# Performance work log

Hardware: AMD Instinct MI355X
Metric: run time of the kernel (lower is better)

## Reference

```python
import jax, jax.numpy as jnp
import numpy as np

B, LQ, LK, D = 8, 2048, 2048, 128
NEG = -100000.0


def setup_inputs() -> dict:
    key = jax.random.key(0)
    kq, kk, kv, km = jax.random.split(key, 4)
    q = jax.random.normal(kq, (B, LQ, D), dtype=jnp.float32)
    k = jax.random.normal(kk, (B, LK, D), dtype=jnp.float32)
    v = jax.random.normal(kv, (B, LK, D), dtype=jnp.float32)
    mask = jax.random.randint(km, (B, LQ, LK), 0, 2, dtype=jnp.int32)
    return {"q": q, "k": k, "v": v, "mask": mask}


def reference(q, k, v, mask):
    # atten_score = q @ k^T / sqrt(d)   [B, Lq, Lk]
    scores = jnp.einsum("bqd,bkd->bqk", q, k) / jnp.sqrt(jnp.float32(q.shape[-1]))
    # mask_mod == 2: additive mask, masked positions pushed to large negative
    scores = scores + mask.astype(jnp.float32) * NEG
    # sigmoid instead of softmax (no normalization across keys)
    attn = jax.nn.sigmoid(scores)
    return jnp.einsum("bqk,bkd->bqd", attn, v)
```

## Files before the change

### kernel.cpp

```cpp
#include <hip/hip_runtime.h>
#include <hip/hip_bf16.h>

#define B_   8
#define LQ_  2048
#define LK_  2048
#define D_   128
#define QBLK 64
#define KBLK 64
#define KSPLIT 2
#define KRANGE (LK_ / KSPLIT)
#define NT    (KRANGE / KBLK)
#define THREADS 512
#define SCALE 0.08838834764831845f

typedef __attribute__((ext_vector_type(8))) __bf16 bf16x8;
typedef __attribute__((ext_vector_type(4))) __bf16 bf16x4;
typedef __attribute__((ext_vector_type(4))) float  f32x4;
typedef __attribute__((ext_vector_type(4))) float  fx4;

#define KS_OFF 0
#define VT_OFF 8192
#define PS_OFF 16384
#define SMEM_ELEMS 21504

__global__ __launch_bounds__(THREADS, 4)
void sigattn_kernel(const float* __restrict__ q, const float* __restrict__ k,
                    const float* __restrict__ v, const int* __restrict__ mask,
                    float* __restrict__ out)
{
    __shared__ __bf16 smem[SMEM_ELEMS];

    const int tid  = threadIdx.x;
    const int lane = tid & 63;
    const int wid  = tid >> 6;
    const int qg   = wid & 3;
    const int kg   = wid >> 2;
    const int l15  = lane & 15;
    const int g    = lane >> 4;

    const int bid  = blockIdx.x;
    const int b    = bid & 7;
    const int rest = bid >> 3;
    const int q0   = (rest >> 1) * QBLK;
    const int ks   = rest & 1;

    const float* qb = q + (size_t)b * LQ_ * D_ + (size_t)q0 * D_;
    const float* kb = k + (size_t)b * LK_ * D_ + (size_t)ks * KRANGE * D_;
    const float* vb = v + (size_t)b * LK_ * D_ + (size_t)ks * KRANGE * D_;
    const int*   mb = mask + (size_t)b * LQ_ * LK_ + (size_t)q0 * LK_ + (size_t)ks * KRANGE;
    float*       ob = out + (size_t)b * LQ_ * D_ + (size_t)q0 * D_;

    __bf16* Ks = smem + KS_OFF;
    __bf16* Vt = smem + VT_OFF;
    __bf16* Ps = smem + PS_OFF + wid * 640;

    const int dv  = tid & 127;
    const int kq8 = tid >> 7;
    const int vswz = ((dv & 7) << 3);

    int mcur[8];

    bf16x8 qfrag[4];
    {
        const float* qrow = qb + (qg * 16 + l15) * D_;
#pragma unroll
        for (int dblk = 0; dblk < 4; ++dblk) {
            fx4 f0 = *(const fx4*)(qrow + dblk * 32 + g * 8);
            fx4 f1 = *(const fx4*)(qrow + dblk * 32 + g * 8 + 4);
            bf16x8 w;
#pragma unroll
            for (int j = 0; j < 4; ++j) { w[j] = (__bf16)f0[j]; w[4 + j] = (__bf16)f1[j]; }
            qfrag[dblk] = w;
        }
    }
#pragma unroll
    for (int i = 0; i < 4; ++i) {
        int idx = tid + i * THREADS;
        int row = idx >> 5, c4 = idx & 31;
        fx4 f = *(const fx4*)(kb + row * D_ + c4 * 4);
        bf16x4 w; w[0]=(__bf16)f[0]; w[1]=(__bf16)f[1]; w[2]=(__bf16)f[2]; w[3]=(__bf16)f[3];
        *(bf16x4*)(Ks + row * 128 + ((c4 * 4) ^ ((row & 7) << 3))) = w;
    }
#pragma unroll
    for (int i = 0; i < 4; ++i) {
        int quad = kq8 + i * 4;
        bf16x4 w;
#pragma unroll
        for (int j = 0; j < 4; ++j) w[j] = (__bf16)vb[(quad * 4 + j) * D_ + dv];
        *(bf16x4*)(Vt + dv * 64 + ((quad * 4) ^ vswz)) = w;
    }
#pragma unroll
    for (int n2 = 0; n2 < 2; ++n2)
#pragma unroll
        for (int r = 0; r < 4; ++r)
            mcur[n2 * 4 + r] = mb[(qg * 16 + 4 * g + r) * LK_ + (kg * 32 + n2 * 16 + l15)];

    f32x4 oacc[8];
#pragma unroll
    for (int nb = 0; nb < 8; ++nb) oacc[nb] = (f32x4){0.f, 0.f, 0.f, 0.f};

    __syncthreads();

    for (int t = 0; t < NT; ++t) {
        const bool more = (t + 1 < NT);

        fx4   kreg[4];
        float vreg[16];
        int   mnxt[8];
        if (more) {
            const int kt = (t + 1) * KBLK;
#pragma unroll
            for (int i = 0; i < 4; ++i) {
                int idx = tid + i * THREADS;
                int row = idx >> 5, c4 = idx & 31;
                kreg[i] = *(const fx4*)(kb + (kt + row) * D_ + c4 * 4);
            }
#pragma unroll
            for (int i = 0; i < 4; ++i) {
                int quad = kq8 + i * 4;
#pragma unroll
                for (int j = 0; j < 4; ++j)
                    vreg[i * 4 + j] = vb[(kt + quad * 4 + j) * D_ + dv];
            }
#pragma unroll
            for (int n2 = 0; n2 < 2; ++n2)
#pragma unroll
                for (int r = 0; r < 4; ++r)
                    mnxt[n2 * 4 + r] = mb[(qg * 16 + 4 * g + r) * LK_ + (kt + kg * 32 + n2 * 16 + l15)];
        }

        f32x4 sacc[2];
        sacc[0] = (f32x4){0.f, 0.f, 0.f, 0.f};
        sacc[1] = (f32x4){0.f, 0.f, 0.f, 0.f};
#pragma unroll
        for (int n2 = 0; n2 < 2; ++n2) {
            const int krow = kg * 32 + n2 * 16 + l15;
            const __bf16* kbase = Ks + krow * 128;
            const int kswz = (krow & 7) << 3;
#pragma unroll
            for (int dblk = 0; dblk < 4; ++dblk) {
                bf16x8 bfr = *(const bf16x8*)(kbase + ((dblk * 32 + g * 8) ^ kswz));
                sacc[n2] = __builtin_amdgcn_mfma_f32_16x16x32_bf16(qfrag[dblk], bfr, sacc[n2], 0, 0, 0);
            }
        }

#pragma unroll
        for (int n2 = 0; n2 < 2; ++n2)
#pragma unroll
            for (int r = 0; r < 4; ++r) {
                float s = sacc[n2][r] * SCALE;
                float p = (mcur[n2 * 4 + r] != 0)
                            ? 0.0f
                            : __builtin_amdgcn_rcpf(1.0f + __expf(-s));
                Ps[(4 * g + r) * 40 + n2 * 16 + l15] = (__bf16)p;
            }

        bf16x8 pfrag = *(const bf16x8*)(Ps + l15 * 40 + g * 8);
#pragma unroll
        for (int nb = 0; nb < 8; ++nb) {
            const int vrow = nb * 16 + l15;
            bf16x8 vfr = *(const bf16x8*)(Vt + vrow * 64 + ((kg * 32 + g * 8) ^ ((vrow & 7) << 3)));
            oacc[nb] = __builtin_amdgcn_mfma_f32_16x16x32_bf16(pfrag, vfr, oacc[nb], 0, 0, 0);
        }

        __syncthreads();

        if (more) {
#pragma unroll
            for (int i = 0; i < 4; ++i) {
                int idx = tid + i * THREADS;
                int row = idx >> 5, c4 = idx & 31;
                bf16x4 w;
                w[0]=(__bf16)kreg[i][0]; w[1]=(__bf16)kreg[i][1];
                w[2]=(__bf16)kreg[i][2]; w[3]=(__bf16)kreg[i][3];
                *(bf16x4*)(Ks + row * 128 + ((c4 * 4) ^ ((row & 7) << 3))) = w;
            }
#pragma unroll
            for (int i = 0; i < 4; ++i) {
                int quad = kq8 + i * 4;
                bf16x4 w;
#pragma unroll
                for (int j = 0; j < 4; ++j) w[j] = (__bf16)vreg[i * 4 + j];
                *(bf16x4*)(Vt + dv * 64 + ((quad * 4) ^ vswz)) = w;
            }
#pragma unroll
            for (int j = 0; j < 8; ++j) mcur[j] = mnxt[j];
        }

        __syncthreads();
    }

    float* red = (float*)smem;
    if (kg == 0) {
#pragma unroll
        for (int nb = 0; nb < 8; ++nb)
#pragma unroll
            for (int r = 0; r < 4; ++r)
                red[(qg * 16 + 4 * g + r) * 128 + nb * 16 + l15] = oacc[nb][r];
    }
    __syncthreads();
    if (kg == 1) {
#pragma unroll
        for (int nb = 0; nb < 8; ++nb)
#pragma unroll
            for (int r = 0; r < 4; ++r) {
                int row = qg * 16 + 4 * g + r;
                float val = red[row * 128 + nb * 16 + l15] + oacc[nb][r];
                atomicAdd(&ob[(size_t)row * D_ + nb * 16 + l15], val);
            }
    }
}

extern "C" void kernel_launch(void* const* d_in, const int* in_sizes, int n_in,
                              void* d_out, int out_size, void* d_ws, size_t ws_size,
                              hipStream_t stream) {
    const float* q    = (const float*)d_in[0];
    const float* k    = (const float*)d_in[1];
    const float* v    = (const float*)d_in[2];
    const int*   mask = (const int*)d_in[3];
    float*       out  = (float*)d_out;

    hipMemsetAsync(out, 0, (size_t)out_size * sizeof(float), stream);

    dim3 grid(B_ * (LQ_ / QBLK) * KSPLIT);
    dim3 block(THREADS);
    sigattn_kernel<<<grid, block, 0, stream>>>(q, k, v, mask, out);
}
```

Measured before the change: 283.0 us.

## Keep P in registers via transposed QK MFMA, vectorize V loads, drop atomics

Swaps the MFMA operand order so the score accumulator already matches the A-fragment layout of the PV MFMA. The P shared-memory round trip is removed and the mask is applied through ballot bitmasks. V tile loads become 2-float vectors with a new swizzle. The split-K atomicAdd plus memset is replaced by plain stores to out and a workspace, followed by a small add kernel. This trades an extra launch and extra global traffic for removing the atomics and LDS traffic.

Measured after the change: 246.7 us. 1.15x faster.

```diff
diff --git a/kernel.cpp b/kernel.cpp
--- a/kernel.cpp
+++ b/kernel.cpp
@@ -17,16 +17,16 @@
 typedef __attribute__((ext_vector_type(4))) __bf16 bf16x4;
 typedef __attribute__((ext_vector_type(4))) float  f32x4;
 typedef __attribute__((ext_vector_type(4))) float  fx4;
+typedef __attribute__((ext_vector_type(2))) float  fx2;
 
 #define KS_OFF 0
 #define VT_OFF 8192
-#define PS_OFF 16384
-#define SMEM_ELEMS 21504
+#define SMEM_ELEMS 16384
 
 __global__ __launch_bounds__(THREADS, 4)
 void sigattn_kernel(const float* __restrict__ q, const float* __restrict__ k,
                     const float* __restrict__ v, const int* __restrict__ mask,
-                    float* __restrict__ out)
+                    float* __restrict__ out, float* __restrict__ ws)
 {
     __shared__ __bf16 smem[SMEM_ELEMS];
 
@@ -49,14 +49,20 @@
     const float* vb = v + (size_t)b * LK_ * D_ + (size_t)ks * KRANGE * D_;
     const int*   mb = mask + (size_t)b * LQ_ * LK_ + (size_t)q0 * LK_ + (size_t)ks * KRANGE;
     float*       ob = out + (size_t)b * LQ_ * D_ + (size_t)q0 * D_;
+    float*       wb = ws  + (size_t)b * LQ_ * D_ + (size_t)q0 * D_;
 
     __bf16* Ks = smem + KS_OFF;
     __bf16* Vt = smem + VT_OFF;
-    __bf16* Ps = smem + PS_OFF + wid * 640;
-
-    const int dv  = tid & 127;
-    const int kq8 = tid >> 7;
-    const int vswz = ((dv & 7) << 3);
+
+    const int dcol  = (tid & 63) * 2;
+    const int kgrp  = tid >> 6;
+    const int vswzq = (tid & 15) << 2;
+    const int colbase = ((kgrp >> 2) << 5) + ((kgrp & 1) << 4) + (((kgrp >> 1) & 1) << 2);
+    const float* vbase = vb + (size_t)(kgrp * 8) * D_ + dcol;
+
+    const int* mbase_p = mb + (qg * 16 + 4 * g) * LK_ + kg * 32 + l15;
+    const int  rsel   = lane & 3;
+    const int  mshift = ((lane & 15) >> 2) * 16 + 4 * (lane >> 4);
 
     int mcur[8];
 
@@ -81,19 +87,25 @@
         bf16x4 w; w[0]=(__bf16)f[0]; w[1]=(__bf16)f[1]; w[2]=(__bf16)f[2]; w[3]=(__bf16)f[3];
         *(bf16x4*)(Ks + row * 128 + ((c4 * 4) ^ ((row & 7) << 3))) = w;
     }
-#pragma unroll
-    for (int i = 0; i < 4; ++i) {
-        int quad = kq8 + i * 4;
-        bf16x4 w;
-#pragma unroll
-        for (int j = 0; j < 4; ++j) w[j] = (__bf16)vb[(quad * 4 + j) * D_ + dv];
-        *(bf16x4*)(Vt + dv * 64 + ((quad * 4) ^ vswz)) = w;
+    {
+        fx2 vld[8];
+#pragma unroll
+        for (int j = 0; j < 8; ++j) vld[j] = *(const fx2*)(vbase + j * D_);
+#pragma unroll
+        for (int dd = 0; dd < 2; ++dd) {
+            bf16x4 lo, hi;
+#pragma unroll
+            for (int j = 0; j < 4; ++j) { lo[j] = (__bf16)vld[j][dd]; hi[j] = (__bf16)vld[4 + j][dd]; }
+            __bf16* vr = Vt + (dcol + dd) * 64;
+            *(bf16x4*)(vr + (colbase ^ vswzq)) = lo;
+            *(bf16x4*)(vr + ((colbase + 8) ^ vswzq)) = hi;
+        }
     }
 #pragma unroll
     for (int n2 = 0; n2 < 2; ++n2)
 #pragma unroll
         for (int r = 0; r < 4; ++r)
-            mcur[n2 * 4 + r] = mb[(qg * 16 + 4 * g + r) * LK_ + (kg * 32 + n2 * 16 + l15)];
+            mcur[n2 * 4 + r] = mbase_p[r * LK_ + n2 * 16];
 
     f32x4 oacc[8];
 #pragma unroll
@@ -104,9 +116,9 @@
     for (int t = 0; t < NT; ++t) {
         const bool more = (t + 1 < NT);
 
-        fx4   kreg[4];
-        float vreg[16];
-        int   mnxt[8];
+        fx4 kreg[4];
+        fx2 vld[8];
+        int mnxt[8];
         if (more) {
             const int kt = (t + 1) * KBLK;
 #pragma unroll
@@ -116,17 +128,12 @@
                 kreg[i] = *(const fx4*)(kb + (kt + row) * D_ + c4 * 4);
             }
 #pragma unroll
-            for (int i = 0; i < 4; ++i) {
-                int quad = kq8 + i * 4;
-#pragma unroll
-                for (int j = 0; j < 4; ++j)
-                    vreg[i * 4 + j] = vb[(kt + quad * 4 + j) * D_ + dv];
-            }
+            for (int j = 0; j < 8; ++j) vld[j] = *(const fx2*)(vbase + (kt + j) * D_);
 #pragma unroll
             for (int n2 = 0; n2 < 2; ++n2)
 #pragma unroll
                 for (int r = 0; r < 4; ++r)
-                    mnxt[n2 * 4 + r] = mb[(qg * 16 + 4 * g + r) * LK_ + (kt + kg * 32 + n2 * 16 + l15)];
+                    mnxt[n2 * 4 + r] = mbase_p[r * LK_ + kt + n2 * 16];
         }
 
         f32x4 sacc[2];
@@ -139,27 +146,45 @@
             const int kswz = (krow & 7) << 3;
 #pragma unroll
             for (int dblk = 0; dblk < 4; ++dblk) {
-                bf16x8 bfr = *(const bf16x8*)(kbase + ((dblk * 32 + g * 8) ^ kswz));
-                sacc[n2] = __builtin_amdgcn_mfma_f32_16x16x32_bf16(qfrag[dblk], bfr, sacc[n2], 0, 0, 0);
-            }
-        }
-
-#pragma unroll
-        for (int n2 = 0; n2 < 2; ++n2)
+                bf16x8 kfr = *(const bf16x8*)(kbase + ((dblk * 32 + g * 8) ^ kswz));
+                sacc[n2] = __builtin_amdgcn_mfma_f32_16x16x32_bf16(kfr, qfrag[dblk], sacc[n2], 0, 0, 0);
+            }
+        }
+
+        unsigned long long bl[8];
+#pragma unroll
+        for (int j = 0; j < 8; ++j) bl[j] = __ballot(mcur[j] != 0);
+        unsigned long long bb0 = (rsel & 2) ? ((rsel & 1) ? bl[3] : bl[2])
+                                            : ((rsel & 1) ? bl[1] : bl[0]);
+        unsigned long long bb1 = (rsel & 2) ? ((rsel & 1) ? bl[7] : bl[6])
+                                            : ((rsel & 1) ? bl[5] : bl[4]);
+        const unsigned int bits0 = (unsigned int)(bb0 >> mshift) & 0xFu;
+        const unsigned int bits1 = (unsigned int)(bb1 >> mshift) & 0xFu;
+
+        bf16x8 pfrag;
+#pragma unroll
+        for (int n2 = 0; n2 < 2; ++n2) {
+            const unsigned int bits = n2 ? bits1 : bits0;
 #pragma unroll
             for (int r = 0; r < 4; ++r) {
                 float s = sacc[n2][r] * SCALE;
-                float p = (mcur[n2 * 4 + r] != 0)
-                            ? 0.0f
-                            : __builtin_amdgcn_rcpf(1.0f + __expf(-s));
-                Ps[(4 * g + r) * 40 + n2 * 16 + l15] = (__bf16)p;
-            }
-
-        bf16x8 pfrag = *(const bf16x8*)(Ps + l15 * 40 + g * 8);
+                float p = __builtin_amdgcn_rcpf(1.0f + __expf(-s));
+                p = ((bits >> r) & 1u) ? 0.0f : p;
+                pfrag[n2 * 4 + r] = (__bf16)p;
+            }
+        }
+
 #pragma unroll
         for (int nb = 0; nb < 8; ++nb) {
-            const int vrow = nb * 16 + l15;
-            bf16x8 vfr = *(const bf16x8*)(Vt + vrow * 64 + ((kg * 32 + g * 8) ^ ((vrow & 7) << 3)));
+            const int row = nb * 16 + l15;
+            const int swz = ((nb & 1) << 5) | ((l15 >> 1) << 2);
+            const __bf16* vrow = Vt + row * 64;
+            const int c = kg * 32 + g * 8;
+            bf16x4 v0 = *(const bf16x4*)(vrow + (c ^ swz));
+            bf16x4 v1 = *(const bf16x4*)(vrow + ((c + 4) ^ swz));
+            bf16x8 vfr;
+#pragma unroll
+            for (int j = 0; j < 4; ++j) { vfr[j] = v0[j]; vfr[4 + j] = v1[j]; }
             oacc[nb] = __builtin_amdgcn_mfma_f32_16x16x32_bf16(pfrag, vfr, oacc[nb], 0, 0, 0);
         }
 
@@ -176,12 +201,13 @@
                 *(bf16x4*)(Ks + row * 128 + ((c4 * 4) ^ ((row & 7) << 3))) = w;
             }
 #pragma unroll
-            for (int i = 0; i < 4; ++i) {
-                int quad = kq8 + i * 4;
-                bf16x4 w;
-#pragma unroll
-                for (int j = 0; j < 4; ++j) w[j] = (__bf16)vreg[i * 4 + j];
-                *(bf16x4*)(Vt + dv * 64 + ((quad * 4) ^ vswz)) = w;
+            for (int dd = 0; dd < 2; ++dd) {
+                bf16x4 lo, hi;
+#pragma unroll
+                for (int j = 0; j < 4; ++j) { lo[j] = (__bf16)vld[j][dd]; hi[j] = (__bf16)vld[4 + j][dd]; }
+                __bf16* vr = Vt + (dcol + dd) * 64;
+                *(bf16x4*)(vr + (colbase ^ vswzq)) = lo;
+                *(bf16x4*)(vr + ((colbase + 8) ^ vswzq)) = hi;
             }
 #pragma unroll
             for (int j = 0; j < 8; ++j) mcur[j] = mnxt[j];
@@ -200,14 +226,27 @@
     }
     __syncthreads();
     if (kg == 1) {
+        float* dst = ks ? wb : ob;
 #pragma unroll
         for (int nb = 0; nb < 8; ++nb)
 #pragma unroll
             for (int r = 0; r < 4; ++r) {
                 int row = qg * 16 + 4 * g + r;
-                float val = red[row * 128 + nb * 16 + l15] + oacc[nb][r];
-                atomicAdd(&ob[(size_t)row * D_ + nb * 16 + l15], val);
-            }
+                dst[(size_t)row * D_ + nb * 16 + l15] =
+                    red[row * 128 + nb * 16 + l15] + oacc[nb][r];
+            }
+    }
+}
+
+__global__ __launch_bounds__(256)
+void reduce_add_kernel(float* __restrict__ out, const float* __restrict__ ws, int n4)
+{
+    int i = blockIdx.x * blockDim.x + threadIdx.x;
+    if (i < n4) {
+        fx4 a = *(const fx4*)(out + i * 4);
+        fx4 c = *(const fx4*)(ws + i * 4);
+        a[0]+=c[0]; a[1]+=c[1]; a[2]+=c[2]; a[3]+=c[3];
+        *(fx4*)(out + i * 4) = a;
     }
 }
 
@@ -219,10 +258,11 @@
     const float* v    = (const float*)d_in[2];
     const int*   mask = (const int*)d_in[3];
     float*       out  = (float*)d_out;
-
-    hipMemsetAsync(out, 0, (size_t)out_size * sizeof(float), stream);
+    float*       ws   = (float*)d_ws;
 
     dim3 grid(B_ * (LQ_ / QBLK) * KSPLIT);
-    dim3 block(THREADS);
-    sigattn_kernel<<<grid, block, 0, stream>>>(q, k, v, mask, out);
+    sigattn_kernel<<<grid, dim3(THREADS), 0, stream>>>(q, k, v, mask, out, ws);
+
+    const int n4 = out_size / 4;
+    reduce_add_kernel<<<(n4 + 255) / 256, 256, 0, stream>>>(out, ws, n4);
 }
```
